# Kernel tuning notes

Hardware: AMD Instinct MI355X
Metric: run time of the kernel (lower is better)

Reference implementation:

```python
import jax, jax.numpy as jnp
import numpy as np

N_POINTS = 2_000_000
OUTPUT_DIM = 8
L_RES = 128
H_RES = 1024


def _to_idx(c, size):
    # c in [-1, 1], align_corners=True mapping to pixel coords
    p = (c + 1.0) * 0.5 * (size - 1)
    i0 = jnp.floor(p)
    w = p - i0  # interpolation weight toward i1
    i0 = jnp.clip(i0.astype(jnp.int32), 0, size - 1)
    i1 = jnp.clip(i0 + 1, 0, size - 1)
    return i0, i1, w


def trilinear_sample(grid, coords):
    # grid: [C, D, H, W]; coords: [N, 3] with (x->W, y->H, z->D); returns [C, N]
    C, D, H, W = grid.shape
    x0, x1, wx = _to_idx(coords[:, 0], W)
    y0, y1, wy = _to_idx(coords[:, 1], H)
    z0, z1, wz = _to_idx(coords[:, 2], D)
    g = lambda zi, yi, xi: grid[:, zi, yi, xi]  # gather -> [C, N]
    out = (g(z0, y0, x0) * ((1 - wz) * (1 - wy) * (1 - wx))
           + g(z0, y0, x1) * ((1 - wz) * (1 - wy) * wx)
           + g(z0, y1, x0) * ((1 - wz) * wy * (1 - wx))
           + g(z0, y1, x1) * ((1 - wz) * wy * wx)
           + g(z1, y0, x0) * (wz * (1 - wy) * (1 - wx))
           + g(z1, y0, x1) * (wz * (1 - wy) * wx)
           + g(z1, y1, x0) * (wz * wy * (1 - wx))
           + g(z1, y1, x1) * (wz * wy * wx))
    return out


def bilinear_sample(plane, coords):
    # plane: [C, H, W]; coords: [N, 2] with (x->W, y->H); returns [C, N]
    C, H, W = plane.shape
    x0, x1, wx = _to_idx(coords[:, 0], W)
    y0, y1, wy = _to_idx(coords[:, 1], H)
    g = lambda yi, xi: plane[:, yi, xi]  # [C, N]
    out = (g(y0, x0) * ((1 - wy) * (1 - wx))
           + g(y0, x1) * ((1 - wy) * wx)
           + g(y1, x0) * (wy * (1 - wx))
           + g(y1, x1) * (wy * wx))
    return out


def setup_inputs() -> dict:
    key = jax.random.key(0)
    k1, k2, k3 = jax.random.split(key, 3)
    xyz = jax.random.uniform(k1, (N_POINTS, 3), dtype=jnp.float32)  # in [0,1) subset of [-1,1]
    L_grid = jax.random.normal(k2, (1, OUTPUT_DIM, L_RES, L_RES, L_RES), dtype=jnp.float32) * 0.1
    H_planes = jax.random.normal(k3, (3, OUTPUT_DIM, H_RES, H_RES), dtype=jnp.float32) * 0.1
    return {"xyz": xyz, "bound": 1, "L_grid": L_grid, "H_planes": H_planes}


def reference(xyz, bound, L_grid, H_planes):
    xyz_norm = xyz / bound  # [N, 3]
    L_out = trilinear_sample(L_grid[0], xyz_norm)  # [C, N]
    H_out = (bilinear_sample(H_planes[0], xyz_norm[:, jnp.array([0, 1])])
             + bilinear_sample(H_planes[1], xyz_norm[:, jnp.array([1, 2])])
             + bilinear_sample(H_planes[2], xyz_norm[:, jnp.array([2, 0])]))
    return (L_out + H_out).T  # [N, C]
```

## Files before the change

kernel.cpp:

```cpp
#include <hip/hip_runtime.h>

#define LRES 128
#define HRES 1024
#define NB 256
#define BTS 1024
#define NBUCK 512
#define RCAP 8192
#define TELEM 2048

static const int LVOX = LRES * LRES * LRES;
static const int PPIX = HRES * HRES;
static const int TV = LVOX + 3 * PPIX;

typedef float f32x4 __attribute__((ext_vector_type(4)));
typedef unsigned u32x4 __attribute__((ext_vector_type(4)));


__device__ __forceinline__ void to_idx(float c, int size, int& i0, int& i1, float& w) {
    float p = (c + 1.0f) * 0.5f * (float)(size - 1);
    float f = floorf(p);
    w = p - f;
    int i = (int)f;
    i0 = min(max(i, 0), size - 1);
    i1 = min(i0 + 1, size - 1);
}

__device__ __forceinline__ unsigned f2bf(float f) {
    unsigned u = __float_as_uint(f);
    return (u + 0x7FFFu + ((u >> 16) & 1u)) >> 16;
}
__device__ __forceinline__ float bflo(unsigned u) { return __uint_as_float(u << 16); }
__device__ __forceinline__ float bfhi(unsigned u) { return __uint_as_float(u & 0xFFFF0000u); }

__device__ __forceinline__ void fma8u(f32x4& a0, f32x4& a1, uint4 q, float w) {
    a0.x = fmaf(bflo(q.x), w, a0.x);
    a0.y = fmaf(bfhi(q.x), w, a0.y);
    a0.z = fmaf(bflo(q.y), w, a0.z);
    a0.w = fmaf(bfhi(q.y), w, a0.w);
    a1.x = fmaf(bflo(q.z), w, a1.x);
    a1.y = fmaf(bfhi(q.z), w, a1.y);
    a1.z = fmaf(bflo(q.w), w, a1.z);
    a1.w = fmaf(bfhi(q.w), w, a1.w);
}

__device__ __forceinline__ unsigned spread3(unsigned x) {
    x &= 0x3FFu;
    x = (x | (x << 16)) & 0x030000FFu;
    x = (x | (x << 8)) & 0x0300F00Fu;
    x = (x | (x << 4)) & 0x030C30C3u;
    x = (x | (x << 2)) & 0x09249249u;
    return x;
}
__device__ __forceinline__ unsigned morton21(float x, float y, float z) {
    int px = min(max((int)(x * 128.f), 0), 127);
    int py = min(max((int)(y * 128.f), 0), 127);
    int pz = min(max((int)(z * 128.f), 0), 127);
    return spread3(px) | (spread3(py) << 1) | (spread3(pz) << 2);
}

__device__ __forceinline__ void gl_lds16(const float* src, float* lds_dst) {
    __builtin_amdgcn_global_load_lds(
        (const __attribute__((address_space(1))) void*)src,
        (__attribute__((address_space(3))) void*)lds_dst, 16, 0, 0);
}

__global__ __launch_bounds__(BTS) void prep_k(const float* __restrict__ xyz,
                                              const int* __restrict__ boundp,
                                              const float* __restrict__ Lg,
                                              const float* __restrict__ Hp,
                                              unsigned* __restrict__ hmat,
                                              u32x4* __restrict__ gclb,
                                              u32x4* __restrict__ pclb, int N) {
    __shared__ float stage[8 * TELEM];
    int b = blockIdx.x;
    if (b < NB) {
        unsigned* h = (unsigned*)stage;
        for (int i = threadIdx.x; i < NBUCK; i += BTS) h[i] = 0u;
        __syncthreads();
        float invb = 1.0f / (float)boundp[0];
        int NG = (N + 3) >> 2;
        for (int g = b * BTS + threadIdx.x; g < NG; g += NB * BTS) {
            int n0 = g << 2;
            if (n0 + 4 <= N) {
                f32x4 qa = *(const f32x4*)(xyz + (size_t)n0 * 3);
                f32x4 qb = *(const f32x4*)(xyz + (size_t)n0 * 3 + 4);
                f32x4 qc = *(const f32x4*)(xyz + (size_t)n0 * 3 + 8);
                atomicAdd(&h[morton21(qa.x * invb, qa.y * invb, qa.z * invb) >> 12], 1u);
                atomicAdd(&h[morton21(qa.w * invb, qb.x * invb, qb.y * invb) >> 12], 1u);
                atomicAdd(&h[morton21(qb.z * invb, qb.w * invb, qc.x * invb) >> 12], 1u);
                atomicAdd(&h[morton21(qc.y * invb, qc.z * invb, qc.w * invb) >> 12], 1u);
            } else {
                for (int n = n0; n < N; ++n) {
                    float x = xyz[(size_t)3 * n + 0] * invb;
                    float y = xyz[(size_t)3 * n + 1] * invb;
                    float z = xyz[(size_t)3 * n + 2] * invb;
                    atomicAdd(&h[morton21(x, y, z) >> 12], 1u);
                }
            }
        }
        __syncthreads();
        for (int i = threadIdx.x; i < NBUCK; i += BTS)
            hmat[(size_t)i * NB + b] = h[i];
    } else {
        int tb = b - NB;
        size_t vbase = (size_t)tb * TELEM;
        const float* srcbase;
        size_t cstride;
        u32x4* dst;
        if (vbase < (size_t)LVOX) {
            srcbase = Lg + vbase;
            cstride = LVOX;
            dst = gclb + vbase;
        } else {
            size_t u = vbase - LVOX;
            int p = (int)(u >> 20);
            size_t r = u & (size_t)(PPIX - 1);
            srcbase = Hp + (size_t)p * 8 * PPIX + r;
            cstride = PPIX;
            dst = pclb + (size_t)p * PPIX + r;
        }
        int wave = threadIdx.x >> 6;
        int lane = threadIdx.x & 63;
        for (int k = wave; k < 64; k += 16) {
            int c = k >> 3, s = k & 7;
            gl_lds16(srcbase + (size_t)c * cstride + s * 256 + lane * 4,
                     &stage[k * 256]);
        }
        __syncthreads();
        int t = threadIdx.x;
#pragma unroll
        for (int e = 0; e < TELEM / BTS; ++e) {
            int v = e * BTS + t;
            unsigned hc[8];
#pragma unroll
            for (int c = 0; c < 8; ++c) hc[c] = f2bf(stage[c * TELEM + v]);
            u32x4 o;
            o.x = hc[0] | (hc[1] << 16);
            o.y = hc[2] | (hc[3] << 16);
            o.z = hc[4] | (hc[5] << 16);
            o.w = hc[6] | (hc[7] << 16);
            dst[v] = o;
        }
    }
}

__global__ __launch_bounds__(1024) void offsets_k(unsigned* __restrict__ hmat,
                                                  unsigned* __restrict__ bb) {
    __shared__ unsigned tot[NBUCK];
    __shared__ unsigned cbase[NBUCK];
    int t = threadIdx.x;
    unsigned run = 0;
    if (t < NBUCK) {
        u32x4* row = (u32x4*)(hmat + (size_t)t * NB);
        for (int ch = 0; ch < NB / 32; ++ch) {
            u32x4 q[8];
#pragma unroll
            for (int k = 0; k < 8; ++k) q[k] = row[ch * 8 + k];
#pragma unroll
            for (int k = 0; k < 8; ++k) {
                unsigned v0 = q[k].x, v1 = q[k].y, v2 = q[k].z, v3 = q[k].w;
                q[k].x = run; run += v0;
                q[k].y = run; run += v1;
                q[k].z = run; run += v2;
                q[k].w = run; run += v3;
                row[ch * 8 + k] = q[k];
            }
        }
        tot[t] = run;
    }
    __syncthreads();
    for (int o = 1; o < NBUCK; o <<= 1) {
        unsigned v = 0;
        if (t < NBUCK && t >= o) v = tot[t - o];
        __syncthreads();
        if (t < NBUCK) tot[t] += v;
        __syncthreads();
    }
    if (t < NBUCK) {
        unsigned excl = tot[t] - run;
        cbase[t] = excl;
        bb[t] = excl;
        if (t == NBUCK - 1) bb[NBUCK] = tot[t];
    }
    __syncthreads();
    u32x4* hm4 = (u32x4*)hmat;
    for (int idx = t; idx < NB * NBUCK / 4; idx += 1024) {
        u32x4 q = hm4[idx];
        unsigned cb = cbase[idx >> 6];
        q.x += cb; q.y += cb; q.z += cb; q.w += cb;
        hm4[idx] = q;
    }
}

__global__ __launch_bounds__(BTS) void scatter_k(const float* __restrict__ xyz,
                                                 const int* __restrict__ boundp,
                                                 const unsigned* __restrict__ hmat,
                                                 float4* __restrict__ s1, int N) {
    __shared__ unsigned cnt[NBUCK];
    int b = blockIdx.x;
    for (int i = threadIdx.x; i < NBUCK; i += BTS)
        cnt[i] = hmat[(size_t)i * NB + b];
    __syncthreads();
    float invb = 1.0f / (float)boundp[0];
    int NG = (N + 3) >> 2;
    for (int g = b * BTS + threadIdx.x; g < NG; g += NB * BTS) {
        int n0 = g << 2;
        if (n0 + 4 <= N) {
            f32x4 qa = *(const f32x4*)(xyz + (size_t)n0 * 3);
            f32x4 qb = *(const f32x4*)(xyz + (size_t)n0 * 3 + 4);
            f32x4 qc = *(const f32x4*)(xyz + (size_t)n0 * 3 + 8);
            {
                float x = qa.x * invb, y = qa.y * invb, z = qa.z * invb;
                unsigned d = atomicAdd(&cnt[morton21(x, y, z) >> 12], 1u);
                s1[d] = make_float4(x, y, z, __int_as_float(n0 + 0));
            }
            {
                float x = qa.w * invb, y = qb.x * invb, z = qb.y * invb;
                unsigned d = atomicAdd(&cnt[morton21(x, y, z) >> 12], 1u);
                s1[d] = make_float4(x, y, z, __int_as_float(n0 + 1));
            }
            {
                float x = qb.z * invb, y = qb.w * invb, z = qc.x * invb;
                unsigned d = atomicAdd(&cnt[morton21(x, y, z) >> 12], 1u);
                s1[d] = make_float4(x, y, z, __int_as_float(n0 + 2));
            }
            {
                float x = qc.y * invb, y = qc.z * invb, z = qc.w * invb;
                unsigned d = atomicAdd(&cnt[morton21(x, y, z) >> 12], 1u);
                s1[d] = make_float4(x, y, z, __int_as_float(n0 + 3));
            }
        } else {
            for (int n = n0; n < N; ++n) {
                float x = xyz[(size_t)3 * n + 0] * invb;
                float y = xyz[(size_t)3 * n + 1] * invb;
                float z = xyz[(size_t)3 * n + 2] * invb;
                unsigned d = atomicAdd(&cnt[morton21(x, y, z) >> 12], 1u);
                s1[d] = make_float4(x, y, z, __int_as_float(n));
            }
        }
    }
}

__global__ __launch_bounds__(1024) void refine_k(const float4* __restrict__ s1,
                                                 const unsigned* __restrict__ bb,
                                                 float4* __restrict__ s2) {
    __shared__ unsigned hist[4096];
    __shared__ unsigned part[1024];
    int b = blockIdx.x;
    unsigned start = bb[b];
    unsigned cnt = bb[b + 1] - start;
    int t = threadIdx.x;
    if (cnt > RCAP) {
        for (unsigned j = t; j < cnt; j += 1024) s2[start + j] = s1[start + j];
        return;
    }
    for (int i = t; i < 4096; i += 1024) hist[i] = 0u;
    __syncthreads();
    float4 rec[RCAP / 1024];
    unsigned key[RCAP / 1024], tick[RCAP / 1024];
#pragma unroll
    for (int k = 0; k < RCAP / 1024; ++k) {
        unsigned j = t + k * 1024u;
        if (j < cnt) {
            rec[k] = s1[start + j];
            key[k] = morton21(rec[k].x, rec[k].y, rec[k].z) & 4095u;
            tick[k] = atomicAdd(&hist[key[k]], 1u);
        }
    }
    __syncthreads();
    unsigned h4[4];
    unsigned s = 0;
#pragma unroll
    for (int k = 0; k < 4; ++k) {
        h4[k] = hist[t * 4 + k];
        s += h4[k];
    }
    part[t] = s;
    __syncthreads();
    for (int o = 1; o < 1024; o <<= 1) {
        unsigned v = (t >= o) ? part[t - o] : 0u;
        __syncthreads();
        part[t] += v;
        __syncthreads();
    }
    unsigned base = part[t] - s;
#pragma unroll
    for (int k = 0; k < 4; ++k) {
        hist[t * 4 + k] = base;
        base += h4[k];
    }
    __syncthreads();
#pragma unroll
    for (int k = 0; k < RCAP / 1024; ++k) {
        unsigned j = t + k * 1024u;
        if (j < cnt) s2[start + hist[key[k]] + tick[k]] = rec[k];
    }
}

__global__ __launch_bounds__(256) void sample_srt(const float4* __restrict__ sorted,
                                                  const uint4* __restrict__ gclb,
                                                  const uint4* __restrict__ pclb,
                                                  float* __restrict__ out, int N) {
    int i = blockIdx.x * blockDim.x + threadIdx.x;
    if (i >= N) return;
    float4 rec = sorted[i];
    float x = rec.x, y = rec.y, z = rec.z;
    int idx = __float_as_int(rec.w);

    int x0, x1, y0, y1, z0, z1;
    float wx, wy, wz;
    to_idx(x, LRES, x0, x1, wx);
    to_idx(y, LRES, y0, y1, wy);
    to_idx(z, LRES, z0, z1, wz);
    const uint4* b00 = gclb + ((size_t)z0 * LRES + y0) * LRES;
    const uint4* b01 = gclb + ((size_t)z0 * LRES + y1) * LRES;
    const uint4* b10 = gclb + ((size_t)z1 * LRES + y0) * LRES;
    const uint4* b11 = gclb + ((size_t)z1 * LRES + y1) * LRES;
    uint4 g0 = b00[x0], g1 = b00[x1], g2 = b01[x0], g3 = b01[x1];
    uint4 g4 = b10[x0], g5 = b10[x1], g6 = b11[x0], g7 = b11[x1];

    const float cw[3] = {x, y, z};
    const float ch[3] = {y, z, x};
    float pww[3], pwh[3];
    uint4 r[12];
#pragma unroll
    for (int p = 0; p < 3; ++p) {
        int w0, w1, h0, h1;
        to_idx(cw[p], HRES, w0, w1, pww[p]);
        to_idx(ch[p], HRES, h0, h1, pwh[p]);
        const uint4* base = pclb + (size_t)p * PPIX;
        const uint4* r0 = base + (size_t)h0 * HRES;
        const uint4* r1 = base + (size_t)h1 * HRES;
        r[4 * p + 0] = r0[w0];
        r[4 * p + 1] = r0[w1];
        r[4 * p + 2] = r1[w0];
        r[4 * p + 3] = r1[w1];
    }

    f32x4 a0 = (f32x4)0.f;
    f32x4 a1 = (f32x4)0.f;
    {
        float ux = 1.f - wx, uy = 1.f - wy, uz = 1.f - wz;
        fma8u(a0, a1, g0, uz * uy * ux);
        fma8u(a0, a1, g1, uz * uy * wx);
        fma8u(a0, a1, g2, uz * wy * ux);
        fma8u(a0, a1, g3, uz * wy * wx);
        fma8u(a0, a1, g4, wz * uy * ux);
        fma8u(a0, a1, g5, wz * uy * wx);
        fma8u(a0, a1, g6, wz * wy * ux);
        fma8u(a0, a1, g7, wz * wy * wx);
    }
#pragma unroll
    for (int p = 0; p < 3; ++p) {
        float ww = pww[p], wh = pwh[p];
        float uw = 1.f - ww, uh = 1.f - wh;
        fma8u(a0, a1, r[4 * p + 0], uh * uw);
        fma8u(a0, a1, r[4 * p + 1], uh * ww);
        fma8u(a0, a1, r[4 * p + 2], wh * uw);
        fma8u(a0, a1, r[4 * p + 3], wh * ww);
    }

    f32x4* o = (f32x4*)(out + (size_t)idx * 8);
    o[0] = a0;
    o[1] = a1;
}

__global__ __launch_bounds__(256) void sample_cf(
    const float* __restrict__ xyz, const int* __restrict__ boundp,
    const float* __restrict__ Lg, const float* __restrict__ Hp,
    float* __restrict__ out, int N) {
    int n = blockIdx.x * blockDim.x + threadIdx.x;
    if (n >= N) return;
    float invb = 1.0f / (float)boundp[0];
    float x = xyz[(size_t)3 * n + 0] * invb;
    float y = xyz[(size_t)3 * n + 1] * invb;
    float z = xyz[(size_t)3 * n + 2] * invb;
    float acc[8];
#pragma unroll
    for (int c = 0; c < 8; ++c) acc[c] = 0.f;
    {
        int x0, x1, y0, y1, z0, z1;
        float wx, wy, wz;
        to_idx(x, LRES, x0, x1, wx);
        to_idx(y, LRES, y0, y1, wy);
        to_idx(z, LRES, z0, z1, wz);
        float ux = 1.f - wx, uy = 1.f - wy, uz = 1.f - wz;
        size_t i8[8];
        i8[0] = ((size_t)z0 * LRES + y0) * LRES + x0;
        i8[1] = ((size_t)z0 * LRES + y0) * LRES + x1;
        i8[2] = ((size_t)z0 * LRES + y1) * LRES + x0;
        i8[3] = ((size_t)z0 * LRES + y1) * LRES + x1;
        i8[4] = ((size_t)z1 * LRES + y0) * LRES + x0;
        i8[5] = ((size_t)z1 * LRES + y0) * LRES + x1;
        i8[6] = ((size_t)z1 * LRES + y1) * LRES + x0;
        i8[7] = ((size_t)z1 * LRES + y1) * LRES + x1;
        float w8[8] = {uz * uy * ux, uz * uy * wx, uz * wy * ux, uz * wy * wx,
                       wz * uy * ux, wz * uy * wx, wz * wy * ux, wz * wy * wx};
#pragma unroll
        for (int c = 0; c < 8; ++c) {
            const float* g = Lg + (size_t)c * LVOX;
            float s = 0.f;
#pragma unroll
            for (int k = 0; k < 8; ++k) s = fmaf(g[i8[k]], w8[k], s);
            acc[c] += s;
        }
    }
    {
        const float cw[3] = {x, y, z};
        const float ch[3] = {y, z, x};
        for (int p = 0; p < 3; ++p) {
            int w0, w1, h0, h1;
            float ww, wh;
            to_idx(cw[p], HRES, w0, w1, ww);
            to_idx(ch[p], HRES, h0, h1, wh);
            float uw = 1.f - ww, uh = 1.f - wh;
            size_t i4[4] = {(size_t)h0 * HRES + w0, (size_t)h0 * HRES + w1,
                            (size_t)h1 * HRES + w0, (size_t)h1 * HRES + w1};
            float w4[4] = {uh * uw, uh * ww, wh * uw, wh * ww};
            const float* pb = Hp + (size_t)p * 8 * PPIX;
#pragma unroll
            for (int c = 0; c < 8; ++c) {
                const float* g = pb + (size_t)c * PPIX;
                float s = 0.f;
#pragma unroll
                for (int k = 0; k < 4; ++k) s = fmaf(g[i4[k]], w4[k], s);
                acc[c] += s;
            }
        }
    }
#pragma unroll
    for (int c = 0; c < 8; ++c) out[(size_t)n * 8 + c] = acc[c];
}

extern "C" void kernel_launch(void* const* d_in, const int* in_sizes, int n_in,
                              void* d_out, int out_size, void* d_ws, size_t ws_size,
                              hipStream_t stream) {
    const float* xyz = (const float*)d_in[0];
    const int* bound = (const int*)d_in[1];
    const float* Lg = (const float*)d_in[2];
    const float* Hp = (const float*)d_in[3];
    float* out = (float*)d_out;
    int N = in_sizes[0] / 3;

    size_t off = 0;
    size_t gclb_b = (size_t)LVOX * 16;
    size_t pclb_b = (size_t)3 * PPIX * 16;
    size_t s1_b = (size_t)N * 16;
    size_t s2_b = (size_t)N * 16;
    size_t hmat_b = (size_t)NB * NBUCK * 4;
    size_t bb_b = (size_t)(NBUCK + 1) * 4;
    size_t need = gclb_b + pclb_b + s1_b + s2_b + hmat_b + bb_b;

    if (ws_size >= need) {
        char* w = (char*)d_ws;
        u32x4* gclb = (u32x4*)(w + off);       off += gclb_b;
        u32x4* pclb = (u32x4*)(w + off);       off += pclb_b;
        float4* s1 = (float4*)(w + off);       off += s1_b;
        float4* s2 = (float4*)(w + off);       off += s2_b;
        unsigned* hmat = (unsigned*)(w + off); off += hmat_b;
        unsigned* bb = (unsigned*)(w + off);

        int prep_blocks = NB + TV / TELEM;
        prep_k<<<prep_blocks, BTS, 0, stream>>>(xyz, bound, Lg, Hp, hmat, gclb, pclb, N);
        offsets_k<<<1, 1024, 0, stream>>>(hmat, bb);
        scatter_k<<<NB, BTS, 0, stream>>>(xyz, bound, hmat, s1, N);
        refine_k<<<NBUCK, 1024, 0, stream>>>(s1, bb, s2);
        sample_srt<<<(N + 255) / 256, 256, 0, stream>>>(s2, (const uint4*)gclb,
                                                        (const uint4*)pclb, out, N);
    } else {
        sample_cf<<<(N + 255) / 256, 256, 0, stream>>>(xyz, bound, Lg, Hp, out, N);
    }
}
```

Measured before the change: 428.2 us.

## Fuse bucket refine sort with sampling, staging sorted records in LDS

Merges the refine sort and the sampling kernel into one kernel. Each block sorts its bucket by local Morton key, scatters the records into an LDS buffer in passes of 4096, and samples directly from LDS, so the s2 global round trip and one launch go away. It also permutes the bucket-to-block mapping to spread nearby buckets across XCDs, and uses nontemporal stores for the output. In exchange, sampling now runs with only 512 blocks of 1024 threads with heavy LDS use and extra syncs, which may reduce occupancy and latency hiding for the gathers. It also re-reads s1 in every pass.

```diff
diff --git a/kernel.cpp b/kernel.cpp
--- a/kernel.cpp
+++ b/kernel.cpp
@@ -62,6 +62,70 @@
     __builtin_amdgcn_global_load_lds(
         (const __attribute__((address_space(1))) void*)src,
         (__attribute__((address_space(3))) void*)lds_dst, 16, 0, 0);
+}
+
+__device__ __forceinline__ void sample_one(float4 rec, const uint4* __restrict__ gclb,
+                                           const uint4* __restrict__ pclb,
+                                           float* __restrict__ out) {
+    float x = rec.x, y = rec.y, z = rec.z;
+    int idx = __float_as_int(rec.w);
+
+    int x0, x1, y0, y1, z0, z1;
+    float wx, wy, wz;
+    to_idx(x, LRES, x0, x1, wx);
+    to_idx(y, LRES, y0, y1, wy);
+    to_idx(z, LRES, z0, z1, wz);
+    const uint4* b00 = gclb + ((size_t)z0 * LRES + y0) * LRES;
+    const uint4* b01 = gclb + ((size_t)z0 * LRES + y1) * LRES;
+    const uint4* b10 = gclb + ((size_t)z1 * LRES + y0) * LRES;
+    const uint4* b11 = gclb + ((size_t)z1 * LRES + y1) * LRES;
+    uint4 g0 = b00[x0], g1 = b00[x1], g2 = b01[x0], g3 = b01[x1];
+    uint4 g4 = b10[x0], g5 = b10[x1], g6 = b11[x0], g7 = b11[x1];
+
+    const float cw[3] = {x, y, z};
+    const float ch[3] = {y, z, x};
+    float pww[3], pwh[3];
+    uint4 r[12];
+#pragma unroll
+    for (int p = 0; p < 3; ++p) {
+        int w0, w1, h0, h1;
+        to_idx(cw[p], HRES, w0, w1, pww[p]);
+        to_idx(ch[p], HRES, h0, h1, pwh[p]);
+        const uint4* base = pclb + (size_t)p * PPIX;
+        const uint4* r0 = base + (size_t)h0 * HRES;
+        const uint4* r1 = base + (size_t)h1 * HRES;
+        r[4 * p + 0] = r0[w0];
+        r[4 * p + 1] = r0[w1];
+        r[4 * p + 2] = r1[w0];
+        r[4 * p + 3] = r1[w1];
+    }
+
+    f32x4 a0 = (f32x4)0.f;
+    f32x4 a1 = (f32x4)0.f;
+    {
+        float ux = 1.f - wx, uy = 1.f - wy, uz = 1.f - wz;
+        fma8u(a0, a1, g0, uz * uy * ux);
+        fma8u(a0, a1, g1, uz * uy * wx);
+        fma8u(a0, a1, g2, uz * wy * ux);
+        fma8u(a0, a1, g3, uz * wy * wx);
+        fma8u(a0, a1, g4, wz * uy * ux);
+        fma8u(a0, a1, g5, wz * uy * wx);
+        fma8u(a0, a1, g6, wz * wy * ux);
+        fma8u(a0, a1, g7, wz * wy * wx);
+    }
+#pragma unroll
+    for (int p = 0; p < 3; ++p) {
+        float ww = pww[p], wh = pwh[p];
+        float uw = 1.f - ww, uh = 1.f - wh;
+        fma8u(a0, a1, r[4 * p + 0], uh * uw);
+        fma8u(a0, a1, r[4 * p + 1], uh * ww);
+        fma8u(a0, a1, r[4 * p + 2], wh * uw);
+        fma8u(a0, a1, r[4 * p + 3], wh * ww);
+    }
+
+    f32x4* o = (f32x4*)(out + (size_t)idx * 8);
+    __builtin_nontemporal_store(a0, o);
+    __builtin_nontemporal_store(a1, o + 1);
 }
 
 __global__ __launch_bounds__(BTS) void prep_k(const float* __restrict__ xyz,
@@ -241,33 +305,43 @@
     }
 }
 
-__global__ __launch_bounds__(1024) void refine_k(const float4* __restrict__ s1,
-                                                 const unsigned* __restrict__ bb,
-                                                 float4* __restrict__ s2) {
-    __shared__ unsigned hist[4096];
-    __shared__ unsigned part[1024];
-    int b = blockIdx.x;
+__global__ __launch_bounds__(1024) void refine_sample_k(const float4* __restrict__ s1,
+                                                        const unsigned* __restrict__ bb,
+                                                        const uint4* __restrict__ gclb,
+                                                        const uint4* __restrict__ pclb,
+                                                        float* __restrict__ out) {
+    __shared__ float4 recbuf[4096];
+    unsigned* hist = (unsigned*)recbuf;
+    unsigned* part = (unsigned*)recbuf + 4096;
+
+    int b0 = blockIdx.x;
+    int b = (b0 & 7) * (NBUCK / 8) + (b0 >> 3);
     unsigned start = bb[b];
     unsigned cnt = bb[b + 1] - start;
     int t = threadIdx.x;
+
     if (cnt > RCAP) {
-        for (unsigned j = t; j < cnt; j += 1024) s2[start + j] = s1[start + j];
+        for (unsigned j = t; j < cnt; j += 1024) sample_one(s1[start + j], gclb, pclb, out);
         return;
     }
+
     for (int i = t; i < 4096; i += 1024) hist[i] = 0u;
     __syncthreads();
-    float4 rec[RCAP / 1024];
-    unsigned key[RCAP / 1024], tick[RCAP / 1024];
+
+    unsigned pk[RCAP / 1024];
 #pragma unroll
     for (int k = 0; k < RCAP / 1024; ++k) {
-        unsigned j = t + k * 1024u;
+        unsigned j = t + (k << 10);
+        pk[k] = 0xFFFFFFFFu;
         if (j < cnt) {
-            rec[k] = s1[start + j];
-            key[k] = morton21(rec[k].x, rec[k].y, rec[k].z) & 4095u;
-            tick[k] = atomicAdd(&hist[key[k]], 1u);
-        }
-    }
-    __syncthreads();
+            float4 r = s1[start + j];
+            unsigned key = morton21(r.x, r.y, r.z) & 4095u;
+            unsigned tick = atomicAdd(&hist[key], 1u);
+            pk[k] = key | (tick << 12);
+        }
+    }
+    __syncthreads();
+
     unsigned h4[4];
     unsigned s = 0;
 #pragma unroll
@@ -290,79 +364,30 @@
         base += h4[k];
     }
     __syncthreads();
-#pragma unroll
-    for (int k = 0; k < RCAP / 1024; ++k) {
-        unsigned j = t + k * 1024u;
-        if (j < cnt) s2[start + hist[key[k]] + tick[k]] = rec[k];
-    }
-}
-
-__global__ __launch_bounds__(256) void sample_srt(const float4* __restrict__ sorted,
-                                                  const uint4* __restrict__ gclb,
-                                                  const uint4* __restrict__ pclb,
-                                                  float* __restrict__ out, int N) {
-    int i = blockIdx.x * blockDim.x + threadIdx.x;
-    if (i >= N) return;
-    float4 rec = sorted[i];
-    float x = rec.x, y = rec.y, z = rec.z;
-    int idx = __float_as_int(rec.w);
-
-    int x0, x1, y0, y1, z0, z1;
-    float wx, wy, wz;
-    to_idx(x, LRES, x0, x1, wx);
-    to_idx(y, LRES, y0, y1, wy);
-    to_idx(z, LRES, z0, z1, wz);
-    const uint4* b00 = gclb + ((size_t)z0 * LRES + y0) * LRES;
-    const uint4* b01 = gclb + ((size_t)z0 * LRES + y1) * LRES;
-    const uint4* b10 = gclb + ((size_t)z1 * LRES + y0) * LRES;
-    const uint4* b11 = gclb + ((size_t)z1 * LRES + y1) * LRES;
-    uint4 g0 = b00[x0], g1 = b00[x1], g2 = b01[x0], g3 = b01[x1];
-    uint4 g4 = b10[x0], g5 = b10[x1], g6 = b11[x0], g7 = b11[x1];
-
-    const float cw[3] = {x, y, z};
-    const float ch[3] = {y, z, x};
-    float pww[3], pwh[3];
-    uint4 r[12];
-#pragma unroll
-    for (int p = 0; p < 3; ++p) {
-        int w0, w1, h0, h1;
-        to_idx(cw[p], HRES, w0, w1, pww[p]);
-        to_idx(ch[p], HRES, h0, h1, pwh[p]);
-        const uint4* base = pclb + (size_t)p * PPIX;
-        const uint4* r0 = base + (size_t)h0 * HRES;
-        const uint4* r1 = base + (size_t)h1 * HRES;
-        r[4 * p + 0] = r0[w0];
-        r[4 * p + 1] = r0[w1];
-        r[4 * p + 2] = r1[w0];
-        r[4 * p + 3] = r1[w1];
-    }
-
-    f32x4 a0 = (f32x4)0.f;
-    f32x4 a1 = (f32x4)0.f;
-    {
-        float ux = 1.f - wx, uy = 1.f - wy, uz = 1.f - wz;
-        fma8u(a0, a1, g0, uz * uy * ux);
-        fma8u(a0, a1, g1, uz * uy * wx);
-        fma8u(a0, a1, g2, uz * wy * ux);
-        fma8u(a0, a1, g3, uz * wy * wx);
-        fma8u(a0, a1, g4, wz * uy * ux);
-        fma8u(a0, a1, g5, wz * uy * wx);
-        fma8u(a0, a1, g6, wz * wy * ux);
-        fma8u(a0, a1, g7, wz * wy * wx);
-    }
-#pragma unroll
-    for (int p = 0; p < 3; ++p) {
-        float ww = pww[p], wh = pwh[p];
-        float uw = 1.f - ww, uh = 1.f - wh;
-        fma8u(a0, a1, r[4 * p + 0], uh * uw);
-        fma8u(a0, a1, r[4 * p + 1], uh * ww);
-        fma8u(a0, a1, r[4 * p + 2], wh * uw);
-        fma8u(a0, a1, r[4 * p + 3], wh * ww);
-    }
-
-    f32x4* o = (f32x4*)(out + (size_t)idx * 8);
-    o[0] = a0;
-    o[1] = a1;
+
+    unsigned pos[RCAP / 1024];
+#pragma unroll
+    for (int k = 0; k < RCAP / 1024; ++k)
+        pos[k] = (pk[k] != 0xFFFFFFFFu) ? (hist[pk[k] & 4095u] + (pk[k] >> 12))
+                                        : 0xFFFFFFFFu;
+    __syncthreads();
+
+    int npass = (int)((cnt + 4095u) >> 12);
+    for (int pass = 0; pass < npass; ++pass) {
+        unsigned lo = (unsigned)pass << 12;
+#pragma unroll
+        for (int k = 0; k < RCAP / 1024; ++k) {
+            unsigned p = pos[k] - lo;
+            if (p < 4096u) recbuf[p] = s1[start + t + (k << 10)];
+        }
+        __syncthreads();
+#pragma unroll
+        for (int k = 0; k < 4; ++k) {
+            unsigned j = lo + t + (k << 10);
+            if (j < cnt) sample_one(recbuf[t + (k << 10)], gclb, pclb, out);
+        }
+        __syncthreads();
+    }
 }
 
 __global__ __launch_bounds__(256) void sample_cf(
@@ -446,17 +471,15 @@
     size_t gclb_b = (size_t)LVOX * 16;
     size_t pclb_b = (size_t)3 * PPIX * 16;
     size_t s1_b = (size_t)N * 16;
-    size_t s2_b = (size_t)N * 16;
     size_t hmat_b = (size_t)NB * NBUCK * 4;
     size_t bb_b = (size_t)(NBUCK + 1) * 4;
-    size_t need = gclb_b + pclb_b + s1_b + s2_b + hmat_b + bb_b;
+    size_t need = gclb_b + pclb_b + s1_b + hmat_b + bb_b;
 
     if (ws_size >= need) {
         char* w = (char*)d_ws;
         u32x4* gclb = (u32x4*)(w + off);       off += gclb_b;
         u32x4* pclb = (u32x4*)(w + off);       off += pclb_b;
         float4* s1 = (float4*)(w + off);       off += s1_b;
-        float4* s2 = (float4*)(w + off);       off += s2_b;
         unsigned* hmat = (unsigned*)(w + off); off += hmat_b;
         unsigned* bb = (unsigned*)(w + off);
 
@@ -464,9 +487,8 @@
         prep_k<<<prep_blocks, BTS, 0, stream>>>(xyz, bound, Lg, Hp, hmat, gclb, pclb, N);
         offsets_k<<<1, 1024, 0, stream>>>(hmat, bb);
         scatter_k<<<NB, BTS, 0, stream>>>(xyz, bound, hmat, s1, N);
-        refine_k<<<NBUCK, 1024, 0, stream>>>(s1, bb, s2);
-        sample_srt<<<(N + 255) / 256, 256, 0, stream>>>(s2, (const uint4*)gclb,
-                                                        (const uint4*)pclb, out, N);
+        refine_sample_k<<<NBUCK, 1024, 0, stream>>>(s1, bb, (const uint4*)gclb,
+                                                    (const uint4*)pclb, out);
     } else {
         sample_cf<<<(N + 255) / 256, 256, 0, stream>>>(xyz, bound, Lg, Hp, out, N);
     }
```

Measured after the change: 553.2 us. +29.2%, slower.
